# Performance work log

Hardware: AMD Instinct MI355X
Metric: run time of the kernel (lower is better)

Reference implementation:

```python
import jax, jax.numpy as jnp
import numpy as np

# bi-degrees (0,0),(1,0),(0,1),(1,1) -> d = (2a+1)*(2b+1)
DEG_DIMS = [1, 3, 3, 9]
P, C = 8192, 256


def setup_inputs() -> dict:
    key = jax.random.key(0)
    kx, k0, k1, k2 = jax.random.split(key, 4)
    scale = 1.0 / np.sqrt(C).astype(np.float32)
    x = jax.random.normal(kx, (P, C, sum(DEG_DIMS)), dtype=jnp.float32)
    # torch.randn(mo, mi) / sqrt(mi); W10 is shared by degrees (1,0) and (0,1)
    W00 = jax.random.normal(k0, (C, C), dtype=jnp.float32) * scale
    W10 = jax.random.normal(k1, (C, C), dtype=jnp.float32) * scale
    W11 = jax.random.normal(k2, (C, C), dtype=jnp.float32) * scale
    return {"x": x, "W00": W00, "W10": W10, "W11": W11}


def reference(x, W00, W10, W11):
    # Weight for each degree segment; (0,1) reuses W10 (parameter tying in GLinear)
    Ws = [W00, W10, W10, W11]
    offsets = np.concatenate([[0], np.cumsum(DEG_DIMS)])
    outs = []
    for W, a, b in zip(Ws, offsets[:-1], offsets[1:]):
        v = x[:, :, a:b]                      # (p, c_in, d_k)
        outs.append(jnp.einsum('oi,pid->pod', W, v))
    out = jnp.concatenate(outs, axis=-1)      # (p, c_out, sum_d)
    # use_skip with matching shared channel -> residual add of input
    return out + x
```

## Files before the change

### kernel.cpp

```cpp
#include <hip/hip_runtime.h>
#include <hip/hip_bf16.h>


#define C_DIM   256
#define D_DIM   16
#define P_TILE  16
#define KC      64
#define LDS_ROW 72

typedef __attribute__((ext_vector_type(8))) short  short8v;
typedef __attribute__((ext_vector_type(4))) float  float4v;
typedef __attribute__((ext_vector_type(4))) unsigned int uint4v;

__device__ __forceinline__ unsigned int pack_bf16x2_rne(float lo, float hi) {
    unsigned int ul = __builtin_bit_cast(unsigned int, lo);
    unsigned int uh = __builtin_bit_cast(unsigned int, hi);
    ul = (ul + 0x7fffu + ((ul >> 16) & 1u)) >> 16;
    uh = (uh + 0x7fffu + ((uh >> 16) & 1u));
    return (ul & 0xffffu) | (uh & 0xffff0000u);
}

__device__ __forceinline__ unsigned int pack_bf16x2_tr(float lo, float hi) {
    return __builtin_amdgcn_perm(__builtin_bit_cast(unsigned int, hi),
                                 __builtin_bit_cast(unsigned int, lo),
                                 0x07060302u);
}

__device__ __forceinline__ short8v load_w_frag(const float* __restrict__ W, int row, int col) {
    const float* p = W + (size_t)row * C_DIM + col;
    float4v a = *(const float4v*)p;
    float4v b = *(const float4v*)(p + 4);
    uint4v u;
    u.x = pack_bf16x2_tr(a.x, a.y);
    u.y = pack_bf16x2_tr(a.z, a.w);
    u.z = pack_bf16x2_tr(b.x, b.y);
    u.w = pack_bf16x2_tr(b.z, b.w);
    return __builtin_bit_cast(short8v, u);
}

__device__ __forceinline__ void glds16(const float* g, float* l) {
    __builtin_amdgcn_global_load_lds(
        (const __attribute__((address_space(1))) void*)g,
        (__attribute__((address_space(3))) void*)l,
        16, 0, 0);
}

__global__ __launch_bounds__(512, 2) void glinear_kernel(
    const float* __restrict__ x, const float* __restrict__ W00,
    const float* __restrict__ W10, const float* __restrict__ W11,
    float* __restrict__ out)
{
    __shared__ __align__(16) float f32s[64 * 256];
    __shared__ __align__(16) unsigned short ls[2][P_TILE * D_DIM * LDS_ROW];

    const int t    = threadIdx.x;
    const int lane = t & 63;
    const int w    = t >> 6;
    const int lm   = lane & 15;
    const int quad = lane >> 4;

    const int ohalf = blockIdx.x & 1;
    const int pbase = (blockIdx.x >> 1) * P_TILE;
    const int obase = ohalf * 128 + w * 16;
    const int orow  = obase + lm;

    const int d4    = t & 3;
    const int ip    = (t >> 2) & 31;
    const int pq    = t >> 7;
    const int i_loc = ip * 2;

    short8v wf[4][2][3];
    #pragma unroll
    for (int ic = 0; ic < 4; ++ic) {
        #pragma unroll
        for (int ks = 0; ks < 2; ++ks) {
            const int col = ic * KC + ks * 32 + quad * 8;
            wf[ic][ks][0] = load_w_frag(W00, orow, col);
            wf[ic][ks][1] = load_w_frag(W10, orow, col);
            wf[ic][ks][2] = load_w_frag(W11, orow, col);
        }
    }
    asm volatile("" ::: "memory");

    auto stage_chunk = [&](int ic) {
        #pragma unroll
        for (int it = 0; it < 4; ++it) {
            const float* src = x + ((size_t)(pbase + pq + it * 4) * C_DIM
                                    + (ic * KC + i_loc)) * D_DIM + d4 * 4;
            glds16(src,         &f32s[((it * 2 + 0) * 8 + w) << 8]);
            glds16(src + D_DIM, &f32s[((it * 2 + 1) * 8 + w) << 8]);
        }
    };

    stage_chunk(0);

    float4v acc[16];
    const float4v fzero = {0.f, 0.f, 0.f, 0.f};
    #pragma unroll
    for (int b = 0; b < 16; ++b) acc[b] = fzero;

    #pragma unroll
    for (int ic = 0; ic < 4; ++ic) {
        const int ib = ic & 1;

        asm volatile("s_waitcnt vmcnt(0)" ::: "memory");

        #pragma unroll
        for (int it = 0; it < 4; ++it) {
            const int p = pq + it * 4;
            float4v a = *(const float4v*)&f32s[((((it * 2 + 0) * 8 + w) << 8)) + lane * 4];
            float4v b = *(const float4v*)&f32s[((((it * 2 + 1) * 8 + w) << 8)) + lane * 4];
            const int g = (i_loc >> 3) ^ (p & 7);
            const int e = i_loc & 7;
            const int base = (p * D_DIM + d4 * 4) * LDS_ROW + g * 8 + e;
            #pragma unroll
            for (int dj = 0; dj < 4; ++dj) {
                *(unsigned int*)(&ls[ib][base + dj * LDS_ROW]) = pack_bf16x2_rne(a[dj], b[dj]);
            }
        }
        __syncthreads();

        if (ic < 3) stage_chunk(ic + 1);
        asm volatile("" ::: "memory");

        #pragma unroll
        for (int ks = 0; ks < 2; ++ks) {
            const int gq = ((ks * 4 + quad) ^ (lm & 7));
            const unsigned short* brow = &ls[ib][lm * D_DIM * LDS_ROW + gq * 8];

            #pragma unroll
            for (int dd = 0; dd < 16; ++dd) {
                short8v xf = *(const short8v*)(brow + dd * LDS_ROW);
                short8v wv = (dd == 0) ? wf[ic][ks][0]
                           : (dd <= 6) ? wf[ic][ks][1]
                                       : wf[ic][ks][2];
                acc[dd] = __builtin_amdgcn_mfma_f32_16x16x32_bf16(xf, wv, acc[dd], 0, 0, 0);
            }
        }
    }

    #pragma unroll
    for (int r = 0; r < 4; ++r) {
        const int p = pbase + quad * 4 + r;
        const int o = obase + lm;
        const size_t off = (size_t)p * (C_DIM * D_DIM) + (size_t)o * D_DIM;
        #pragma unroll
        for (int g = 0; g < 4; ++g) {
            float4v v;
            v.x = acc[g * 4 + 0][r];
            v.y = acc[g * 4 + 1][r];
            v.z = acc[g * 4 + 2][r];
            v.w = acc[g * 4 + 3][r];
            float4v xr = *(const float4v*)(x + off + g * 4);
            *(float4v*)(out + off + g * 4) = v + xr;
        }
    }
}

extern "C" void kernel_launch(void* const* d_in, const int* in_sizes, int n_in,
                              void* d_out, int out_size, void* d_ws, size_t ws_size,
                              hipStream_t stream) {
    const float* x   = (const float*)d_in[0];
    const float* W00 = (const float*)d_in[1];
    const float* W10 = (const float*)d_in[2];
    const float* W11 = (const float*)d_in[3];
    float* out = (float*)d_out;

    dim3 grid(1024);
    dim3 block(512);
    hipLaunchKernelGGL(glinear_kernel, grid, block, 0, stream, x, W00, W10, W11, out);
}
```

Baseline: 304.5 us.

## Persist blocks over four point tiles and prepack bf16 weight fragments

```diff
diff --git a/kernel.cpp b/kernel.cpp
--- a/kernel.cpp
+++ b/kernel.cpp
@@ -7,6 +7,9 @@
 #define P_TILE  16
 #define KC      64
 #define LDS_ROW 72
+#define UNITS   4
+#define NFRAG   (2 * 8 * 24 * 64)
+#define WS_NEEDED (NFRAG * 16)
 
 typedef __attribute__((ext_vector_type(8))) short  short8v;
 typedef __attribute__((ext_vector_type(4))) float  float4v;
@@ -45,10 +48,39 @@
         16, 0, 0);
 }
 
+__global__ __launch_bounds__(256, 4) void init_w_pack(
+    const float* __restrict__ W00, const float* __restrict__ W10,
+    const float* __restrict__ W11, uint4v* __restrict__ ws)
+{
+    const int tid = blockIdx.x * 256 + threadIdx.x;
+    if (tid >= NFRAG) return;
+    const int l   = tid & 63;
+    int idx = tid >> 6;
+    const int f  = idx % 24;
+    idx /= 24;
+    const int w  = idx & 7;
+    const int oh = idx >> 3;
+    const int mat = f % 3;
+    const int ks  = (f / 3) & 1;
+    const int ic  = f / 6;
+    const float* Wm = (mat == 0) ? W00 : (mat == 1) ? W10 : W11;
+    const int row = oh * 128 + w * 16 + (l & 15);
+    const int col = ic * KC + ks * 32 + (l >> 4) * 8;
+    const float* p = Wm + (size_t)row * C_DIM + col;
+    float4v a = *(const float4v*)p;
+    float4v b = *(const float4v*)(p + 4);
+    uint4v u;
+    u.x = pack_bf16x2_rne(a.x, a.y);
+    u.y = pack_bf16x2_rne(a.z, a.w);
+    u.z = pack_bf16x2_rne(b.x, b.y);
+    u.w = pack_bf16x2_rne(b.z, b.w);
+    ws[tid] = u;
+}
+
 __global__ __launch_bounds__(512, 2) void glinear_kernel(
     const float* __restrict__ x, const float* __restrict__ W00,
     const float* __restrict__ W10, const float* __restrict__ W11,
-    float* __restrict__ out)
+    float* __restrict__ out, const short8v* __restrict__ wpack, int use_ws)
 {
     __shared__ __align__(16) float f32s[64 * 256];
     __shared__ __align__(16) unsigned short ls[2][P_TILE * D_DIM * LDS_ROW];
@@ -59,9 +91,9 @@
     const int lm   = lane & 15;
     const int quad = lane >> 4;
 
-    const int ohalf = blockIdx.x & 1;
-    const int pbase = (blockIdx.x >> 1) * P_TILE;
-    const int obase = ohalf * 128 + w * 16;
+    const int oh    = blockIdx.x & 1;
+    const int pg    = blockIdx.x >> 1;
+    const int obase = oh * 128 + w * 16;
     const int orow  = obase + lm;
 
     const int d4    = t & 3;
@@ -70,89 +102,104 @@
     const int i_loc = ip * 2;
 
     short8v wf[4][2][3];
-    #pragma unroll
-    for (int ic = 0; ic < 4; ++ic) {
-        #pragma unroll
-        for (int ks = 0; ks < 2; ++ks) {
-            const int col = ic * KC + ks * 32 + quad * 8;
-            wf[ic][ks][0] = load_w_frag(W00, orow, col);
-            wf[ic][ks][1] = load_w_frag(W10, orow, col);
-            wf[ic][ks][2] = load_w_frag(W11, orow, col);
-        }
+    if (use_ws && wpack != nullptr) {
+        const short8v* wbase = wpack + ((size_t)(oh * 8 + w) * 24) * 64 + lane;
+        #pragma unroll
+        for (int ic = 0; ic < 4; ++ic)
+            #pragma unroll
+            for (int ks = 0; ks < 2; ++ks)
+                #pragma unroll
+                for (int mat = 0; mat < 3; ++mat)
+                    wf[ic][ks][mat] = wbase[(size_t)(ic * 6 + ks * 3 + mat) * 64];
+    } else {
+        #pragma unroll
+        for (int ic = 0; ic < 4; ++ic)
+            #pragma unroll
+            for (int ks = 0; ks < 2; ++ks) {
+                const int col = ic * KC + ks * 32 + quad * 8;
+                wf[ic][ks][0] = load_w_frag(W00, orow, col);
+                wf[ic][ks][1] = load_w_frag(W10, orow, col);
+                wf[ic][ks][2] = load_w_frag(W11, orow, col);
+            }
     }
     asm volatile("" ::: "memory");
 
-    auto stage_chunk = [&](int ic) {
+    auto stage_chunk = [&](int pb, int ic) {
         #pragma unroll
         for (int it = 0; it < 4; ++it) {
-            const float* src = x + ((size_t)(pbase + pq + it * 4) * C_DIM
+            const float* src = x + ((size_t)(pb + pq + it * 4) * C_DIM
                                     + (ic * KC + i_loc)) * D_DIM + d4 * 4;
             glds16(src,         &f32s[((it * 2 + 0) * 8 + w) << 8]);
             glds16(src + D_DIM, &f32s[((it * 2 + 1) * 8 + w) << 8]);
         }
     };
 
-    stage_chunk(0);
-
-    float4v acc[16];
-    const float4v fzero = {0.f, 0.f, 0.f, 0.f};
-    #pragma unroll
-    for (int b = 0; b < 16; ++b) acc[b] = fzero;
-
-    #pragma unroll
-    for (int ic = 0; ic < 4; ++ic) {
-        const int ib = ic & 1;
-
-        asm volatile("s_waitcnt vmcnt(0)" ::: "memory");
-
-        #pragma unroll
-        for (int it = 0; it < 4; ++it) {
-            const int p = pq + it * 4;
-            float4v a = *(const float4v*)&f32s[((((it * 2 + 0) * 8 + w) << 8)) + lane * 4];
-            float4v b = *(const float4v*)&f32s[((((it * 2 + 1) * 8 + w) << 8)) + lane * 4];
-            const int g = (i_loc >> 3) ^ (p & 7);
-            const int e = i_loc & 7;
-            const int base = (p * D_DIM + d4 * 4) * LDS_ROW + g * 8 + e;
-            #pragma unroll
-            for (int dj = 0; dj < 4; ++dj) {
-                *(unsigned int*)(&ls[ib][base + dj * LDS_ROW]) = pack_bf16x2_rne(a[dj], b[dj]);
+    stage_chunk(pg * UNITS * P_TILE, 0);
+
+    for (int u = 0; u < UNITS; ++u) {
+        const int pbase = (pg * UNITS + u) * P_TILE;
+
+        float4v acc[16];
+        const float4v fzero = {0.f, 0.f, 0.f, 0.f};
+        #pragma unroll
+        for (int b = 0; b < 16; ++b) acc[b] = fzero;
+
+        #pragma unroll
+        for (int ic = 0; ic < 4; ++ic) {
+            const int ib = ic & 1;
+
+            asm volatile("s_waitcnt vmcnt(0)" ::: "memory");
+
+            #pragma unroll
+            for (int it = 0; it < 4; ++it) {
+                const int p = pq + it * 4;
+                float4v a = *(const float4v*)&f32s[((((it * 2 + 0) * 8 + w) << 8)) + lane * 4];
+                float4v b = *(const float4v*)&f32s[((((it * 2 + 1) * 8 + w) << 8)) + lane * 4];
+                const int g = (i_loc >> 3) ^ (p & 7);
+                const int e = i_loc & 7;
+                const int base = (p * D_DIM + d4 * 4) * LDS_ROW + g * 8 + e;
+                #pragma unroll
+                for (int dj = 0; dj < 4; ++dj) {
+                    *(unsigned int*)(&ls[ib][base + dj * LDS_ROW]) = pack_bf16x2_rne(a[dj], b[dj]);
+                }
+            }
+            __syncthreads();
+
+            if (ic < 3)               stage_chunk(pbase, ic + 1);
+            else if (u < UNITS - 1)   stage_chunk(pbase + P_TILE, 0);
+            asm volatile("" ::: "memory");
+
+            #pragma unroll
+            for (int ks = 0; ks < 2; ++ks) {
+                const int gq = ((ks * 4 + quad) ^ (lm & 7));
+                const unsigned short* brow = &ls[ib][lm * D_DIM * LDS_ROW + gq * 8];
+
+                #pragma unroll
+                for (int dd = 0; dd < 16; ++dd) {
+                    short8v xf = *(const short8v*)(brow + dd * LDS_ROW);
+                    short8v wv = (dd == 0) ? wf[ic][ks][0]
+                               : (dd <= 6) ? wf[ic][ks][1]
+                                           : wf[ic][ks][2];
+                    acc[dd] = __builtin_amdgcn_mfma_f32_16x16x32_bf16(xf, wv, acc[dd], 0, 0, 0);
+                }
             }
         }
-        __syncthreads();
-
-        if (ic < 3) stage_chunk(ic + 1);
-        asm volatile("" ::: "memory");
-
-        #pragma unroll
-        for (int ks = 0; ks < 2; ++ks) {
-            const int gq = ((ks * 4 + quad) ^ (lm & 7));
-            const unsigned short* brow = &ls[ib][lm * D_DIM * LDS_ROW + gq * 8];
-
-            #pragma unroll
-            for (int dd = 0; dd < 16; ++dd) {
-                short8v xf = *(const short8v*)(brow + dd * LDS_ROW);
-                short8v wv = (dd == 0) ? wf[ic][ks][0]
-                           : (dd <= 6) ? wf[ic][ks][1]
-                                       : wf[ic][ks][2];
-                acc[dd] = __builtin_amdgcn_mfma_f32_16x16x32_bf16(xf, wv, acc[dd], 0, 0, 0);
-            }
-        }
-    }
-
-    #pragma unroll
-    for (int r = 0; r < 4; ++r) {
-        const int p = pbase + quad * 4 + r;
-        const int o = obase + lm;
-        const size_t off = (size_t)p * (C_DIM * D_DIM) + (size_t)o * D_DIM;
-        #pragma unroll
-        for (int g = 0; g < 4; ++g) {
-            float4v v;
-            v.x = acc[g * 4 + 0][r];
-            v.y = acc[g * 4 + 1][r];
-            v.z = acc[g * 4 + 2][r];
-            v.w = acc[g * 4 + 3][r];
-            float4v xr = *(const float4v*)(x + off + g * 4);
-            *(float4v*)(out + off + g * 4) = v + xr;
+
+        #pragma unroll
+        for (int r = 0; r < 4; ++r) {
+            const int p = pbase + quad * 4 + r;
+            const int o = obase + lm;
+            const size_t off = (size_t)p * (C_DIM * D_DIM) + (size_t)o * D_DIM;
+            #pragma unroll
+            for (int g = 0; g < 4; ++g) {
+                float4v v;
+                v.x = acc[g * 4 + 0][r];
+                v.y = acc[g * 4 + 1][r];
+                v.z = acc[g * 4 + 2][r];
+                v.w = acc[g * 4 + 3][r];
+                float4v xr = *(const float4v*)(x + off + g * 4);
+                *(float4v*)(out + off + g * 4) = v + xr;
+            }
         }
     }
 }
@@ -166,7 +213,11 @@
     const float* W11 = (const float*)d_in[3];
     float* out = (float*)d_out;
 
-    dim3 grid(1024);
-    dim3 block(512);
-    hipLaunchKernelGGL(glinear_kernel, grid, block, 0, stream, x, W00, W10, W11, out);
-}
+    const int use_ws = (d_ws != nullptr && ws_size >= WS_NEEDED) ? 1 : 0;
+    if (use_ws) {
+        hipLaunchKernelGGL(init_w_pack, dim3(96), dim3(256), 0, stream,
+                           W00, W10, W11, (uint4v*)d_ws);
+    }
+    hipLaunchKernelGGL(glinear_kernel, dim3(256), dim3(512), 0, stream,
+                       x, W00, W10, W11, out, (const short8v*)d_ws, use_ws);
+}
```

Measured after the change: 279.5 us. 8.2% less time.
